# Kernel optimization log

Hardware: AMD Instinct MI355X
Metric: run time of the kernel (lower is better)

The kernel has to match this reference:

```python
import jax, jax.numpy as jnp
import numpy as np

NUM_HEADS = 16
D_K = 8  # == n_qubits


def setup_inputs() -> dict:
    key = jax.random.key(0)
    k1, k2, k3 = jax.random.split(key, 3)
    x = jax.random.normal(k1, (4, 2048, 128), dtype=jnp.float32)
    # trainable RX angles, one per qubit (tq.RX has_params=True)
    theta = jax.random.normal(k2, (D_K,), dtype=jnp.float32)
    # out_proj: Linear(embed_dim, embed_dim, bias=False)
    w_out = jax.random.normal(k3, (128, 128), dtype=jnp.float32) * (1.0 / np.sqrt(128.0))
    return {"x": x, "theta": theta, "w_out": w_out}


def quantum_features(x, theta):
    # x: [b, s, e]. Per head of size d_k: encode RX(x_i), trainable RX(theta_i)
    # (composes to RX(x_i + theta_i)), CNOT ladder [i, i+1], measure PauliZ.
    # Heisenberg picture: Z_w -> Z_0...Z_w, so <Z_w> = prod_{i<=w} cos(x_i + theta_i).
    b, s, e = x.shape
    heads = x.reshape(b, s, NUM_HEADS, D_K)
    return jnp.cumprod(jnp.cos(heads + theta), axis=-1)  # [b, s, h, d_k]


def reference(x, theta, w_out):
    b, s, e = x.shape
    # q == k == v: same shared q_layer applied to the same x three times.
    qkv = quantum_features(x, theta)            # [b, s, h, d_k]
    q = qkv.transpose(0, 2, 1, 3)               # [b, h, s, d_k]
    scores = jnp.einsum('bhqd,bhkd->bhqk', q, q) / np.sqrt(D_K)
    attn = jax.nn.softmax(scores, axis=-1)      # dropout is identity at eval
    out = jnp.einsum('bhqk,bhkd->bhqd', attn, q)
    out = out.transpose(0, 2, 1, 3).reshape(b, s, e)
    return out @ w_out.T
```

## Files before the change

### kernel.cpp

```cpp
#include <hip/hip_runtime.h>

#define BATCH 4
#define SEQ   2048
#define EMB   128
#define NH    16
#define DK    8

#define QSCALE 0.510069726f

typedef _Float16 v4h  __attribute__((ext_vector_type(4)));
typedef _Float16 v8h  __attribute__((ext_vector_type(8)));
typedef __fp16   v2fp __attribute__((ext_vector_type(2)));
typedef float    v4f  __attribute__((ext_vector_type(4)));
typedef float    v16f __attribute__((ext_vector_type(16)));

#define CHUNK  512
#define NCH    (SEQ / CHUNK)
#define VTP    520

__launch_bounds__(256, 4)
__global__ void attn_kernel(const float* __restrict__ x,
                            const float* __restrict__ theta,
                            _Float16* __restrict__ Ah ) {
  __shared__ __align__(16) _Float16 Kl[CHUNK * 8];
  __shared__ __align__(16) _Float16 VT[10][VTP];

  const int tid = threadIdx.x;
  const int L   = tid & 63;
  const int ln  = L & 31;
  const int hf  = L >> 5;
  const int wv  = tid >> 6;
  const int bh     = blockIdx.x >> 4;
  const int qchunk = blockIdx.x & 15;
  const int qb     = qchunk * 128 + wv * 32;
  const int b = bh >> 4;
  const int h = bh & 15;

  float th[DK];
#pragma unroll
  for (int i = 0; i < DK; ++i) th[i] = theta[i];

  for (int i = tid; i < VTP; i += 256) {
    VT[8][i] = (_Float16)1.0f;
    VT[9][i] = (_Float16)0.0f;
  }

  const int c0 = qchunk >> 2;
  const int mrow = (ln < 9) ? ln : 9;
  const float* xb = x + (size_t)b * SEQ * EMB + h * DK;

  float4 pa0, pa1, pb0, pb1;
  {
    const float* xp = xb + (size_t)(c0 * CHUNK + tid) * EMB;
    pa0 = *(const float4*)(xp);
    pa1 = *(const float4*)(xp + 4);
    pb0 = *(const float4*)(xp + 256 * EMB);
    pb1 = *(const float4*)(xp + 256 * EMB + 4);
  }

  v8h qf = {0, 0, 0, 0, 0, 0, 0, 0};
  v16f acc;
#pragma unroll
  for (int i = 0; i < 16; ++i) acc[i] = 0.f;
  v16f zf;
#pragma unroll
  for (int i = 0; i < 16; ++i) zf[i] = 0.f;

  for (int cc = 0; cc < NCH; ++cc) {
    if (cc) __syncthreads();

    {
      float r0[8], r1[8];
      r0[0] = __cosf(pa0.x + th[0]);
      r0[1] = r0[0] * __cosf(pa0.y + th[1]);
      r0[2] = r0[1] * __cosf(pa0.z + th[2]);
      r0[3] = r0[2] * __cosf(pa0.w + th[3]);
      r0[4] = r0[3] * __cosf(pa1.x + th[4]);
      r0[5] = r0[4] * __cosf(pa1.y + th[5]);
      r0[6] = r0[5] * __cosf(pa1.z + th[6]);
      r0[7] = r0[6] * __cosf(pa1.w + th[7]);
      r1[0] = __cosf(pb0.x + th[0]);
      r1[1] = r1[0] * __cosf(pb0.y + th[1]);
      r1[2] = r1[1] * __cosf(pb0.z + th[2]);
      r1[3] = r1[2] * __cosf(pb0.w + th[3]);
      r1[4] = r1[3] * __cosf(pb1.x + th[4]);
      r1[5] = r1[4] * __cosf(pb1.y + th[5]);
      r1[6] = r1[5] * __cosf(pb1.z + th[6]);
      r1[7] = r1[6] * __cosf(pb1.w + th[7]);

      _Float16 h0[8], h1[8];
#pragma unroll
      for (int i = 0; i < 8; ++i) { h0[i] = (_Float16)r0[i]; h1[i] = (_Float16)r1[i]; }

      union { v4h v[2]; float4 f; } u0, u1;
      u0.v[0] = (v4h){h0[0], h0[1], h0[2], h0[3]};
      u0.v[1] = (v4h){h0[4], h0[5], h0[6], h0[7]};
      u1.v[0] = (v4h){h1[0], h1[1], h1[2], h1[3]};
      u1.v[1] = (v4h){h1[4], h1[5], h1[6], h1[7]};
      *(float4*)&Kl[tid * 8]         = u0.f;
      *(float4*)&Kl[(tid + 256) * 8] = u1.f;

      const int j0 = tid, j1 = tid + 256;
      const int col0 = (j0 & ~15) | (j0 & 3) | ((j0 & 4) << 1) | ((j0 & 8) >> 1);
      const int col1 = (j1 & ~15) | (j1 & 3) | ((j1 & 4) << 1) | ((j1 & 8) >> 1);
#pragma unroll
      for (int d = 0; d < 8; ++d) {
        VT[d][col0] = h0[d];
        VT[d][col1] = h1[d];
      }
    }
    __syncthreads();

    if (cc + 1 < NCH) {
      const int cn = (c0 + cc + 1) & (NCH - 1);
      const float* xp = xb + (size_t)(cn * CHUNK + tid) * EMB;
      pa0 = *(const float4*)(xp);
      pa1 = *(const float4*)(xp + 4);
      pb0 = *(const float4*)(xp + 256 * EMB);
      pb1 = *(const float4*)(xp + 256 * EMB + 4);
    }

    if (cc == 0 && hf == 0) {
      const int ql = (qchunk & 3) * 128 + wv * 32 + ln;
      v8h qv = *(const v8h*)&Kl[ql * 8];
      const _Float16 qs = (_Float16)QSCALE;
      const v8h qsc = {qs, qs, qs, qs, qs, qs, qs, qs};
      qf = qv * qsc;
    }

    v8h kf_next = *(const v8h*)&Kl[ln * 8];
#pragma unroll 2
    for (int kb = 0; kb < CHUNK / 32; ++kb) {
      const v8h kf = kf_next;
      const v16f s = __builtin_amdgcn_mfma_f32_32x32x16_f16(kf, qf, zf, 0, 0, 0);
      if (kb + 1 < CHUNK / 32)
        kf_next = *(const v8h*)&Kl[((kb + 1) * 32 + ln) * 8];
      const v8h vt0 = *(const v8h*)&VT[mrow][kb * 32 + hf * 8];
      const v8h vt1 = *(const v8h*)&VT[mrow][kb * 32 + 16 + hf * 8];
      union { v2fp p[4]; v8h v; } p0, p1;
#pragma unroll
      for (int i = 0; i < 4; ++i) {
        p0.p[i] = __builtin_amdgcn_cvt_pkrtz(
            __builtin_amdgcn_exp2f(s[2 * i]),
            __builtin_amdgcn_exp2f(s[2 * i + 1]));
        p1.p[i] = __builtin_amdgcn_cvt_pkrtz(
            __builtin_amdgcn_exp2f(s[8 + 2 * i]),
            __builtin_amdgcn_exp2f(s[8 + 2 * i + 1]));
      }
      acc = __builtin_amdgcn_mfma_f32_32x32x16_f16(vt0, p0.v, acc, 0, 0, 0);
      acc = __builtin_amdgcn_mfma_f32_32x32x16_f16(vt1, p1.v, acc, 0, 0, 0);
    }
  }

  {
    const float den = __shfl(acc[4], ln, 64);
    const float inv = 1.0f / den;
    const int qrow = qb + ln;
    v4h o = {(_Float16)(acc[0] * inv), (_Float16)(acc[1] * inv),
             (_Float16)(acc[2] * inv), (_Float16)(acc[3] * inv)};
    *(v4h*)(Ah + ((size_t)b * SEQ + qrow) * EMB + h * DK + hf * 4) = o;
  }
}

__launch_bounds__(256, 4)
__global__ void proj_kernel(const _Float16* __restrict__ Ah,
                            const float* __restrict__ W,
                            float* __restrict__ out) {
  __shared__ __align__(16) _Float16 Ahs[64][136];
  __shared__ __align__(16) _Float16 Whs[64][136];

  const int tid  = threadIdx.x;
  const int L    = tid & 63;
  const int wv   = tid >> 6;
  const int quad = L >> 4;
  const int ln   = L & 15;
  const int rowbase = blockIdx.x * 64;
  const int colbase = blockIdx.y * 64;

#pragma unroll
  for (int it = 0; it < 4; ++it) {
    const int idx = it * 256 + tid;
    const int r  = idx >> 4;
    const int c8 = idx & 15;
    *(uint4*)&Ahs[r][c8 * 8] =
        *(const uint4*)(Ah + (size_t)(rowbase + r) * EMB + c8 * 8);
  }
#pragma unroll
  for (int it = 0; it < 8; ++it) {
    const int idx = it * 256 + tid;
    const int n  = idx >> 5;
    const int c4 = idx & 31;
    const float4 w = *(const float4*)(W + (size_t)(colbase + n) * EMB + c4 * 4);
    v4h wh = {(_Float16)w.x, (_Float16)w.y, (_Float16)w.z, (_Float16)w.w};
    *(v4h*)&Whs[n][c4 * 4] = wh;
  }
  __syncthreads();

  v4f acc[4];
#pragma unroll
  for (int nt = 0; nt < 4; ++nt) acc[nt] = (v4f){0.f, 0.f, 0.f, 0.f};

#pragma unroll
  for (int k8 = 0; k8 < 8; ++k8) {
    const v4h af = *(const v4h*)&Ahs[wv * 16 + ln][k8 * 16 + quad * 4];
#pragma unroll
    for (int nt = 0; nt < 4; ++nt) {
      const v4h bf = *(const v4h*)&Whs[nt * 16 + ln][k8 * 16 + quad * 4];
      acc[nt] = __builtin_amdgcn_mfma_f32_16x16x16f16(af, bf, acc[nt], 0, 0, 0);
    }
  }

#pragma unroll
  for (int nt = 0; nt < 4; ++nt) {
    const int col = colbase + nt * 16 + ln;
#pragma unroll
    for (int r = 0; r < 4; ++r) {
      out[(size_t)(rowbase + wv * 16 + quad * 4 + r) * EMB + col] = acc[nt][r];
    }
  }
}

extern "C" void kernel_launch(void* const* d_in, const int* in_sizes, int n_in,
                              void* d_out, int out_size, void* d_ws, size_t ws_size,
                              hipStream_t stream) {
  const float* x     = (const float*)d_in[0];
  const float* theta = (const float*)d_in[1];
  const float* w_out = (const float*)d_in[2];
  float* out = (float*)d_out;

  _Float16* Ah = (_Float16*)d_ws;

  attn_kernel<<<dim3(1024), dim3(256), 0, stream>>>(x, theta, Ah);

  proj_kernel<<<dim3((BATCH * SEQ) / 64, 2), dim3(256), 0, stream>>>(Ah, w_out, out);
}
```

Baseline: 95.07 us.

## Split attention keys across two blocks and merge partial sums in projection

Each attention block now handles half of the key sequence, which doubles the grid to 2048 blocks and raises the occupancy hint to 8 blocks per SM. Queries are computed directly from x instead of being read from the shared key tile. Unnormalized partial outputs and softmax denominators are written in fp32 and combined and normalized in the projection kernel's load stage. This gives more parallelism and halves the per-block loop length, at the cost of extra global writes and reads of fp32 partials.

```diff
diff --git a/kernel.cpp b/kernel.cpp
--- a/kernel.cpp
+++ b/kernel.cpp
@@ -15,13 +15,13 @@
 typedef float    v16f __attribute__((ext_vector_type(16)));
 
 #define CHUNK  512
-#define NCH    (SEQ / CHUNK)
 #define VTP    520
 
-__launch_bounds__(256, 4)
+__launch_bounds__(256, 8)
 __global__ void attn_kernel(const float* __restrict__ x,
                             const float* __restrict__ theta,
-                            _Float16* __restrict__ Ah ) {
+                            float* __restrict__ PO   ,
+                            float* __restrict__ DEN  ) {
   __shared__ __align__(16) _Float16 Kl[CHUNK * 8];
   __shared__ __align__(16) _Float16 VT[10][VTP];
 
@@ -30,8 +30,10 @@
   const int ln  = L & 31;
   const int hf  = L >> 5;
   const int wv  = tid >> 6;
-  const int bh     = blockIdx.x >> 4;
-  const int qchunk = blockIdx.x & 15;
+  const int bx  = blockIdx.x;
+  const int bh     = bx >> 5;
+  const int qchunk = (bx >> 1) & 15;
+  const int kh     = bx & 1;
   const int qb     = qchunk * 128 + wv * 32;
   const int b = bh >> 4;
   const int h = bh & 15;
@@ -45,13 +47,12 @@
     VT[9][i] = (_Float16)0.0f;
   }
 
-  const int c0 = qchunk >> 2;
   const int mrow = (ln < 9) ? ln : 9;
   const float* xb = x + (size_t)b * SEQ * EMB + h * DK;
 
   float4 pa0, pa1, pb0, pb1;
   {
-    const float* xp = xb + (size_t)(c0 * CHUNK + tid) * EMB;
+    const float* xp = xb + (size_t)(kh * 2 * CHUNK + tid) * EMB;
     pa0 = *(const float4*)(xp);
     pa1 = *(const float4*)(xp + 4);
     pb0 = *(const float4*)(xp + 256 * EMB);
@@ -59,6 +60,28 @@
   }
 
   v8h qf = {0, 0, 0, 0, 0, 0, 0, 0};
+  if (hf == 0) {
+    const float* xq = xb + (size_t)(qb + ln) * EMB;
+    const float4 q0 = *(const float4*)(xq);
+    const float4 q1 = *(const float4*)(xq + 4);
+    float r[8];
+    r[0] = __cosf(q0.x + th[0]);
+    r[1] = r[0] * __cosf(q0.y + th[1]);
+    r[2] = r[1] * __cosf(q0.z + th[2]);
+    r[3] = r[2] * __cosf(q0.w + th[3]);
+    r[4] = r[3] * __cosf(q1.x + th[4]);
+    r[5] = r[4] * __cosf(q1.y + th[5]);
+    r[6] = r[5] * __cosf(q1.z + th[6]);
+    r[7] = r[6] * __cosf(q1.w + th[7]);
+    _Float16 hq[8];
+#pragma unroll
+    for (int i = 0; i < 8; ++i) hq[i] = (_Float16)r[i];
+    const _Float16 qs = (_Float16)QSCALE;
+    const v8h qsc = {qs, qs, qs, qs, qs, qs, qs, qs};
+    const v8h qv  = {hq[0], hq[1], hq[2], hq[3], hq[4], hq[5], hq[6], hq[7]};
+    qf = qv * qsc;
+  }
+
   v16f acc;
 #pragma unroll
   for (int i = 0; i < 16; ++i) acc[i] = 0.f;
@@ -66,7 +89,7 @@
 #pragma unroll
   for (int i = 0; i < 16; ++i) zf[i] = 0.f;
 
-  for (int cc = 0; cc < NCH; ++cc) {
+  for (int cc = 0; cc < 2; ++cc) {
     if (cc) __syncthreads();
 
     {
@@ -111,21 +134,12 @@
     }
     __syncthreads();
 
-    if (cc + 1 < NCH) {
-      const int cn = (c0 + cc + 1) & (NCH - 1);
-      const float* xp = xb + (size_t)(cn * CHUNK + tid) * EMB;
+    if (cc == 0) {
+      const float* xp = xb + (size_t)((kh * 2 + 1) * CHUNK + tid) * EMB;
       pa0 = *(const float4*)(xp);
       pa1 = *(const float4*)(xp + 4);
       pb0 = *(const float4*)(xp + 256 * EMB);
       pb1 = *(const float4*)(xp + 256 * EMB + 4);
-    }
-
-    if (cc == 0 && hf == 0) {
-      const int ql = (qchunk & 3) * 128 + wv * 32 + ln;
-      v8h qv = *(const v8h*)&Kl[ql * 8];
-      const _Float16 qs = (_Float16)QSCALE;
-      const v8h qsc = {qs, qs, qs, qs, qs, qs, qs, qs};
-      qf = qv * qsc;
     }
 
     v8h kf_next = *(const v8h*)&Kl[ln * 8];
@@ -153,17 +167,17 @@
   }
 
   {
-    const float den = __shfl(acc[4], ln, 64);
-    const float inv = 1.0f / den;
     const int qrow = qb + ln;
-    v4h o = {(_Float16)(acc[0] * inv), (_Float16)(acc[1] * inv),
-             (_Float16)(acc[2] * inv), (_Float16)(acc[3] * inv)};
-    *(v4h*)(Ah + ((size_t)b * SEQ + qrow) * EMB + h * DK + hf * 4) = o;
+    const size_t pbase = ((((size_t)kh * BATCH + b) * NH + h) * SEQ + qrow);
+    const float4 o = {acc[0], acc[1], acc[2], acc[3]};
+    *(float4*)&PO[pbase * 8 + (size_t)hf * 4] = o;
+    if (hf == 0) DEN[pbase] = acc[4];
   }
 }
 
 __launch_bounds__(256, 4)
-__global__ void proj_kernel(const _Float16* __restrict__ Ah,
+__global__ void proj_kernel(const float* __restrict__ PO,
+                            const float* __restrict__ DEN,
                             const float* __restrict__ W,
                             float* __restrict__ out) {
   __shared__ __align__(16) _Float16 Ahs[64][136];
@@ -180,10 +194,24 @@
 #pragma unroll
   for (int it = 0; it < 4; ++it) {
     const int idx = it * 256 + tid;
-    const int r  = idx >> 4;
-    const int c8 = idx & 15;
-    *(uint4*)&Ahs[r][c8 * 8] =
-        *(const uint4*)(Ah + (size_t)(rowbase + r) * EMB + c8 * 8);
+    const int hh = idx >> 6;
+    const int r  = idx & 63;
+    const size_t srow = (size_t)rowbase + r;
+    const int bb = (int)(srow >> 11);
+    const int sl = (int)(srow & 2047);
+    const size_t p0 = ((((size_t)0 * BATCH + bb) * NH + hh) * SEQ + sl);
+    const size_t p1 = ((((size_t)1 * BATCH + bb) * NH + hh) * SEQ + sl);
+    const float4 a0 = *(const float4*)&PO[p0 * 8];
+    const float4 b0 = *(const float4*)&PO[p0 * 8 + 4];
+    const float4 a1 = *(const float4*)&PO[p1 * 8];
+    const float4 b1 = *(const float4*)&PO[p1 * 8 + 4];
+    const float inv = 1.0f / (DEN[p0] + DEN[p1]);
+    const v4h lo = {(_Float16)((a0.x + a1.x) * inv), (_Float16)((a0.y + a1.y) * inv),
+                    (_Float16)((a0.z + a1.z) * inv), (_Float16)((a0.w + a1.w) * inv)};
+    const v4h hi = {(_Float16)((b0.x + b1.x) * inv), (_Float16)((b0.y + b1.y) * inv),
+                    (_Float16)((b0.z + b1.z) * inv), (_Float16)((b0.w + b1.w) * inv)};
+    *(v4h*)&Ahs[r][hh * 8]     = lo;
+    *(v4h*)&Ahs[r][hh * 8 + 4] = hi;
   }
 #pragma unroll
   for (int it = 0; it < 8; ++it) {
@@ -228,9 +256,10 @@
   const float* w_out = (const float*)d_in[2];
   float* out = (float*)d_out;
 
-  _Float16* Ah = (_Float16*)d_ws;
-
-  attn_kernel<<<dim3(1024), dim3(256), 0, stream>>>(x, theta, Ah);
-
-  proj_kernel<<<dim3((BATCH * SEQ) / 64, 2), dim3(256), 0, stream>>>(Ah, w_out, out);
+  float* PO  = (float*)d_ws;
+  float* DEN = PO + (size_t)2 * BATCH * NH * SEQ * 8;
+
+  attn_kernel<<<dim3(2048), dim3(256), 0, stream>>>(x, theta, PO, DEN);
+
+  proj_kernel<<<dim3((BATCH * SEQ) / 64, 2), dim3(256), 0, stream>>>(PO, DEN, w_out, out);
 }
```

Measured after the change: 101.1 us. 6.4% more time.

## Process two query tiles per wave in attention and shrink projection tiles

Applied to the files above, without the earlier changes.

Each attention wave now handles 64 query rows (two 32-row MFMA tiles) instead of 32. Each K/V chunk loaded and encoded into LDS is therefore reused across twice as many queries, and the grid halves to 512 blocks, which cuts the redundant recomputation of quantum features per block. The projection kernel switches to 32-row tiles with a 2x2 wave split, doubling its grid to improve parallelism. In exchange, attention register pressure rises and fewer blocks are available to fill the CUs.

```diff
diff --git a/kernel.cpp b/kernel.cpp
--- a/kernel.cpp
+++ b/kernel.cpp
@@ -30,9 +30,8 @@
   const int ln  = L & 31;
   const int hf  = L >> 5;
   const int wv  = tid >> 6;
-  const int bh     = blockIdx.x >> 4;
-  const int qchunk = blockIdx.x & 15;
-  const int qb     = qchunk * 128 + wv * 32;
+  const int bh  = blockIdx.x >> 3;
+  const int qg  = blockIdx.x & 7;
   const int b = bh >> 4;
   const int h = bh & 15;
 
@@ -45,7 +44,7 @@
     VT[9][i] = (_Float16)0.0f;
   }
 
-  const int c0 = qchunk >> 2;
+  const int c0 = qg >> 1;
   const int mrow = (ln < 9) ? ln : 9;
   const float* xb = x + (size_t)b * SEQ * EMB + h * DK;
 
@@ -58,13 +57,11 @@
     pb1 = *(const float4*)(xp + 256 * EMB + 4);
   }
 
-  v8h qf = {0, 0, 0, 0, 0, 0, 0, 0};
-  v16f acc;
-#pragma unroll
-  for (int i = 0; i < 16; ++i) acc[i] = 0.f;
-  v16f zf;
-#pragma unroll
-  for (int i = 0; i < 16; ++i) zf[i] = 0.f;
+  v8h qf0 = {0, 0, 0, 0, 0, 0, 0, 0};
+  v8h qf1 = {0, 0, 0, 0, 0, 0, 0, 0};
+  v16f acc0, acc1, zf;
+#pragma unroll
+  for (int i = 0; i < 16; ++i) { acc0[i] = 0.f; acc1[i] = 0.f; zf[i] = 0.f; }
 
   for (int cc = 0; cc < NCH; ++cc) {
     if (cc) __syncthreads();
@@ -121,44 +118,61 @@
     }
 
     if (cc == 0 && hf == 0) {
-      const int ql = (qchunk & 3) * 128 + wv * 32 + ln;
-      v8h qv = *(const v8h*)&Kl[ql * 8];
+      const int ql = (qg & 1) * 256 + wv * 64 + ln;
       const _Float16 qs = (_Float16)QSCALE;
       const v8h qsc = {qs, qs, qs, qs, qs, qs, qs, qs};
-      qf = qv * qsc;
-    }
-
-    v8h kf_next = *(const v8h*)&Kl[ln * 8];
+      qf0 = *(const v8h*)&Kl[ql * 8] * qsc;
+      qf1 = *(const v8h*)&Kl[(ql + 32) * 8] * qsc;
+    }
+
+    v8h kf = *(const v8h*)&Kl[ln * 8];
 #pragma unroll 2
     for (int kb = 0; kb < CHUNK / 32; ++kb) {
-      const v8h kf = kf_next;
-      const v16f s = __builtin_amdgcn_mfma_f32_32x32x16_f16(kf, qf, zf, 0, 0, 0);
-      if (kb + 1 < CHUNK / 32)
-        kf_next = *(const v8h*)&Kl[((kb + 1) * 32 + ln) * 8];
+      const v8h kf_n = *(const v8h*)&Kl[((((kb + 1) & 15) * 32) + ln) * 8];
+      const v16f s0 = __builtin_amdgcn_mfma_f32_32x32x16_f16(kf, qf0, zf, 0, 0, 0);
+      const v16f s1 = __builtin_amdgcn_mfma_f32_32x32x16_f16(kf, qf1, zf, 0, 0, 0);
       const v8h vt0 = *(const v8h*)&VT[mrow][kb * 32 + hf * 8];
       const v8h vt1 = *(const v8h*)&VT[mrow][kb * 32 + 16 + hf * 8];
-      union { v2fp p[4]; v8h v; } p0, p1;
+      union { v2fp p[4]; v8h v; } a0, a1, b0, b1;
 #pragma unroll
       for (int i = 0; i < 4; ++i) {
-        p0.p[i] = __builtin_amdgcn_cvt_pkrtz(
-            __builtin_amdgcn_exp2f(s[2 * i]),
-            __builtin_amdgcn_exp2f(s[2 * i + 1]));
-        p1.p[i] = __builtin_amdgcn_cvt_pkrtz(
-            __builtin_amdgcn_exp2f(s[8 + 2 * i]),
-            __builtin_amdgcn_exp2f(s[8 + 2 * i + 1]));
+        a0.p[i] = __builtin_amdgcn_cvt_pkrtz(
+            __builtin_amdgcn_exp2f(s0[2 * i]),
+            __builtin_amdgcn_exp2f(s0[2 * i + 1]));
+        a1.p[i] = __builtin_amdgcn_cvt_pkrtz(
+            __builtin_amdgcn_exp2f(s0[8 + 2 * i]),
+            __builtin_amdgcn_exp2f(s0[8 + 2 * i + 1]));
       }
-      acc = __builtin_amdgcn_mfma_f32_32x32x16_f16(vt0, p0.v, acc, 0, 0, 0);
-      acc = __builtin_amdgcn_mfma_f32_32x32x16_f16(vt1, p1.v, acc, 0, 0, 0);
+      acc0 = __builtin_amdgcn_mfma_f32_32x32x16_f16(vt0, a0.v, acc0, 0, 0, 0);
+      acc0 = __builtin_amdgcn_mfma_f32_32x32x16_f16(vt1, a1.v, acc0, 0, 0, 0);
+#pragma unroll
+      for (int i = 0; i < 4; ++i) {
+        b0.p[i] = __builtin_amdgcn_cvt_pkrtz(
+            __builtin_amdgcn_exp2f(s1[2 * i]),
+            __builtin_amdgcn_exp2f(s1[2 * i + 1]));
+        b1.p[i] = __builtin_amdgcn_cvt_pkrtz(
+            __builtin_amdgcn_exp2f(s1[8 + 2 * i]),
+            __builtin_amdgcn_exp2f(s1[8 + 2 * i + 1]));
+      }
+      acc1 = __builtin_amdgcn_mfma_f32_32x32x16_f16(vt0, b0.v, acc1, 0, 0, 0);
+      acc1 = __builtin_amdgcn_mfma_f32_32x32x16_f16(vt1, b1.v, acc1, 0, 0, 0);
+      kf = kf_n;
     }
   }
 
   {
-    const float den = __shfl(acc[4], ln, 64);
-    const float inv = 1.0f / den;
-    const int qrow = qb + ln;
-    v4h o = {(_Float16)(acc[0] * inv), (_Float16)(acc[1] * inv),
-             (_Float16)(acc[2] * inv), (_Float16)(acc[3] * inv)};
-    *(v4h*)(Ah + ((size_t)b * SEQ + qrow) * EMB + h * DK + hf * 4) = o;
+    const int qrow0 = qg * 256 + wv * 64 + ln;
+    const float den0 = __shfl(acc0[4], ln, 64);
+    const float inv0 = 1.0f / den0;
+    v4h o0 = {(_Float16)(acc0[0] * inv0), (_Float16)(acc0[1] * inv0),
+              (_Float16)(acc0[2] * inv0), (_Float16)(acc0[3] * inv0)};
+    *(v4h*)(Ah + ((size_t)b * SEQ + qrow0) * EMB + h * DK + hf * 4) = o0;
+
+    const float den1 = __shfl(acc1[4], ln, 64);
+    const float inv1 = 1.0f / den1;
+    v4h o1 = {(_Float16)(acc1[0] * inv1), (_Float16)(acc1[1] * inv1),
+              (_Float16)(acc1[2] * inv1), (_Float16)(acc1[3] * inv1)};
+    *(v4h*)(Ah + ((size_t)b * SEQ + qrow0 + 32) * EMB + h * DK + hf * 4) = o1;
   }
 }
 
@@ -166,7 +180,7 @@
 __global__ void proj_kernel(const _Float16* __restrict__ Ah,
                             const float* __restrict__ W,
                             float* __restrict__ out) {
-  __shared__ __align__(16) _Float16 Ahs[64][136];
+  __shared__ __align__(16) _Float16 Ahs[32][136];
   __shared__ __align__(16) _Float16 Whs[64][136];
 
   const int tid  = threadIdx.x;
@@ -174,11 +188,11 @@
   const int wv   = tid >> 6;
   const int quad = L >> 4;
   const int ln   = L & 15;
-  const int rowbase = blockIdx.x * 64;
+  const int rowbase = blockIdx.x * 32;
   const int colbase = blockIdx.y * 64;
 
 #pragma unroll
-  for (int it = 0; it < 4; ++it) {
+  for (int it = 0; it < 2; ++it) {
     const int idx = it * 256 + tid;
     const int r  = idx >> 4;
     const int c8 = idx & 15;
@@ -196,26 +210,29 @@
   }
   __syncthreads();
 
-  v4f acc[4];
-#pragma unroll
-  for (int nt = 0; nt < 4; ++nt) acc[nt] = (v4f){0.f, 0.f, 0.f, 0.f};
+  const int rowoff = (wv & 1) * 16;
+  const int coloff = (wv >> 1) * 32;
+
+  v4f acc[2];
+#pragma unroll
+  for (int nt = 0; nt < 2; ++nt) acc[nt] = (v4f){0.f, 0.f, 0.f, 0.f};
 
 #pragma unroll
   for (int k8 = 0; k8 < 8; ++k8) {
-    const v4h af = *(const v4h*)&Ahs[wv * 16 + ln][k8 * 16 + quad * 4];
-#pragma unroll
-    for (int nt = 0; nt < 4; ++nt) {
-      const v4h bf = *(const v4h*)&Whs[nt * 16 + ln][k8 * 16 + quad * 4];
+    const v4h af = *(const v4h*)&Ahs[rowoff + ln][k8 * 16 + quad * 4];
+#pragma unroll
+    for (int nt = 0; nt < 2; ++nt) {
+      const v4h bf = *(const v4h*)&Whs[coloff + nt * 16 + ln][k8 * 16 + quad * 4];
       acc[nt] = __builtin_amdgcn_mfma_f32_16x16x16f16(af, bf, acc[nt], 0, 0, 0);
     }
   }
 
 #pragma unroll
-  for (int nt = 0; nt < 4; ++nt) {
-    const int col = colbase + nt * 16 + ln;
+  for (int nt = 0; nt < 2; ++nt) {
+    const int col = colbase + coloff + nt * 16 + ln;
 #pragma unroll
     for (int r = 0; r < 4; ++r) {
-      out[(size_t)(rowbase + wv * 16 + quad * 4 + r) * EMB + col] = acc[nt][r];
+      out[(size_t)(rowbase + rowoff + quad * 4 + r) * EMB + col] = acc[nt][r];
     }
   }
 }
@@ -230,7 +247,7 @@
 
   _Float16* Ah = (_Float16*)d_ws;
 
-  attn_kernel<<<dim3(1024), dim3(256), 0, stream>>>(x, theta, Ah);
-
-  proj_kernel<<<dim3((BATCH * SEQ) / 64, 2), dim3(256), 0, stream>>>(Ah, w_out, out);
+  attn_kernel<<<dim3(512), dim3(256), 0, stream>>>(x, theta, Ah);
+
+  proj_kernel<<<dim3((BATCH * SEQ) / 32, 2), dim3(256), 0, stream>>>(Ah, w_out, out);
 }
```

New measurement: 93.72 us. No clear change (-1.4%).
